# Performance work log

Hardware: AMD Instinct MI355X
Metric: run time of the kernel (lower is better)

The kernel has to match this reference:

```python
import jax, jax.numpy as jnp
import numpy as np

N_HEAD = 16

def setup_inputs() -> dict:
    key = jax.random.key(0)
    k1, k2, k3, k4 = jax.random.split(key, 4)
    B, S, D = 4, 1024, 1024
    x = jax.random.normal(k1, (B, S, D), dtype=jnp.float32)
    # 0/1 float mask: cls_mask[:,0] overrides row 0, cls_mask[:,1] overrides col 0
    cls_mask = jax.random.randint(k2, (B, 2, S), 0, 2).astype(jnp.float32)
    w_attn = jax.random.normal(k3, (D, 3 * D), dtype=jnp.float32) * 0.02
    b_attn = jnp.zeros((3 * D,), dtype=jnp.float32)
    w_proj = jax.random.normal(k4, (D, D), dtype=jnp.float32) * 0.02
    b_proj = jnp.zeros((D,), dtype=jnp.float32)
    return {"x": x, "cls_mask": cls_mask, "w_attn": w_attn, "b_attn": b_attn,
            "w_proj": w_proj, "b_proj": b_proj}

def reference(x, cls_mask, w_attn, b_attn, w_proj, b_proj):
    B, S, D = x.shape
    H = N_HEAD
    hd = D // H
    cm = jnp.broadcast_to(jnp.tril(jnp.ones((S, S), x.dtype))[None, None], (B, 1, S, S))
    cm = cm.at[:, :, 0, :].set(cls_mask[:, 0][:, None, :])
    cm = cm.at[:, :, :, 0].set(cls_mask[:, 1][:, None, :])
    qkv = x @ w_attn + b_attn                      # [B,S,3D]
    q, k, v = jnp.split(qkv, 3, axis=-1)
    split_heads = lambda t: t.reshape(B, S, H, hd).transpose(0, 2, 1, 3)  # [B,H,S,hd]
    q, k, v = split_heads(q), split_heads(k), split_heads(v)
    w = jnp.einsum('bhqd,bhkd->bhqk', q, k) / jnp.sqrt(jnp.asarray(hd, x.dtype))
    w = w * cm - 10000.0 * (1.0 - cm)
    w = jax.nn.softmax(w, axis=-1)
    a = jnp.einsum('bhqk,bhkd->bhqd', w, v)
    a = a.transpose(0, 2, 1, 3).reshape(B, S, D)   # merge heads
    a = a @ w_proj + b_proj
    present = jnp.stack((k, v))                    # [2,B,H,S,hd]
    return a, present
```

## Files before the change

kernel.cpp:

```cpp
#include <hip/hip_runtime.h>
#include <hip/hip_bf16.h>

typedef __bf16 bf16x8 __attribute__((ext_vector_type(8)));
typedef float f32x4 __attribute__((ext_vector_type(4)));

__device__ __forceinline__ f32x4 mfma16(bf16x8 a, bf16x8 b, f32x4 c) {
    return __builtin_amdgcn_mfma_f32_16x16x32_bf16(a, b, c, 0, 0, 0);
}

typedef __attribute__((address_space(1))) const unsigned int GUInt;
typedef __attribute__((address_space(3))) unsigned int LUInt;
__device__ __forceinline__ void gl_lds16(const void* g, void* l) {
    __builtin_amdgcn_global_load_lds((GUInt*)g, (LUInt*)l, 16, 0, 0);
}

__device__ __forceinline__ int psw(int row, int bir) {
    return row * 128 + (bir ^ ((row & 7) << 4));
}

__global__ __launch_bounds__(256) void cast_kernel(const float* __restrict__ in,
                                                   __hip_bfloat16* __restrict__ out, int n4) {
    int i = blockIdx.x * 256 + threadIdx.x;
    if (i >= n4) return;
    float4 v = reinterpret_cast<const float4*>(in)[i];
    __hip_bfloat16 o[4];
    o[0] = __float2bfloat16(v.x); o[1] = __float2bfloat16(v.y);
    o[2] = __float2bfloat16(v.z); o[3] = __float2bfloat16(v.w);
    *reinterpret_cast<uint2*>(&out[i * 4]) = *reinterpret_cast<const uint2*>(o);
}

__global__ __launch_bounds__(256) void transpose_cast_kernel(const float* __restrict__ in,
                                                             __hip_bfloat16* __restrict__ out,
                                                             int K, int N) {
    __shared__ float tile[64][65];
    int kt = blockIdx.x, nt = blockIdx.y;
    int c = threadIdx.x & 63, r4 = threadIdx.x >> 6;
#pragma unroll
    for (int i = 0; i < 16; ++i) {
        int r = i * 4 + r4;
        tile[r][c] = in[(kt * 64 + r) * N + nt * 64 + c];
    }
    __syncthreads();
#pragma unroll
    for (int i = 0; i < 16; ++i) {
        int rr = i * 4 + r4;
        out[(nt * 64 + rr) * K + kt * 64 + c] = __float2bfloat16(tile[c][rr]);
    }
}

template <int EPI>
__global__ __launch_bounds__(256) void gemm_kernel(
    const __hip_bfloat16* __restrict__ A, const __hip_bfloat16* __restrict__ Bt,
    const float* __restrict__ bias, int M, int N, int K,
    float* __restrict__ Cf,
    __hip_bfloat16* __restrict__ Qbf, __hip_bfloat16* __restrict__ Kbf,
    __hip_bfloat16* __restrict__ VbfT, float* __restrict__ present) {
    __shared__ __align__(16) char As[128 * 128];
    __shared__ __align__(16) char Bs[128 * 128];
    const int tid = threadIdx.x;
    const int lane = tid & 63;
    const int w = tid >> 6;
    const int lr = lane & 15;
    const int lg = lane >> 4;
    const int wm = (w >> 1) * 64;
    const int wn = (w & 1) * 64;
    const int bm = blockIdx.y, bn = blockIdx.x;
    const int swz = (lr & 7) << 4;

    const int srow = tid >> 3;
    const int ccs = ((tid & 7) * 16) ^ ((srow & 7) << 4);
    const char* aBase = (const char*)A + ((size_t)(bm * 128 + srow) * K) * 2 + ccs;
    const char* bBase = (const char*)Bt + ((size_t)(bn * 128 + srow) * K) * 2 + ccs;

    f32x4 zv = {0.f, 0.f, 0.f, 0.f};
    f32x4 acc[4][4];
#pragma unroll
    for (int i = 0; i < 4; ++i)
#pragma unroll
        for (int j = 0; j < 4; ++j) acc[i][j] = zv;

    for (int k0 = 0; k0 < K; k0 += 64) {
#pragma unroll
        for (int j = 0; j < 4; ++j) {
            gl_lds16(aBase + ((size_t)j * 32 * K + k0) * 2, &As[j * 4096 + tid * 16]);
            gl_lds16(bBase + ((size_t)j * 32 * K + k0) * 2, &Bs[j * 4096 + tid * 16]);
        }
        __syncthreads();
#pragma unroll
        for (int kk = 0; kk < 2; ++kk) {
            bf16x8 af[4], bfr[4];
#pragma unroll
            for (int mt = 0; mt < 4; ++mt)
                af[mt] = *reinterpret_cast<const bf16x8*>(
                    &As[(wm + mt * 16 + lr) * 128 + ((kk * 64 + lg * 16) ^ swz)]);
#pragma unroll
            for (int nt = 0; nt < 4; ++nt)
                bfr[nt] = *reinterpret_cast<const bf16x8*>(
                    &Bs[(wn + nt * 16 + lr) * 128 + ((kk * 64 + lg * 16) ^ swz)]);
#pragma unroll
            for (int mt = 0; mt < 4; ++mt)
#pragma unroll
                for (int nt = 0; nt < 4; ++nt)
                    acc[mt][nt] = mfma16(af[mt], bfr[nt], acc[mt][nt]);
        }
        __syncthreads();
    }

#pragma unroll
    for (int mt = 0; mt < 4; ++mt) {
        const int mbase = bm * 128 + wm + mt * 16 + lg * 4;
        const int bb = mbase >> 10, s0 = mbase & 1023;
#pragma unroll
        for (int nt = 0; nt < 4; ++nt) {
            const int n = bn * 128 + wn + nt * 16 + lr;
            const float bias_n = bias[n];
            float v[4];
#pragma unroll
            for (int r = 0; r < 4; ++r) v[r] = acc[mt][nt][r] + bias_n;
            if (EPI == 0) {
#pragma unroll
                for (int r = 0; r < 4; ++r) Cf[(size_t)(mbase + r) * N + n] = v[r];
            } else {
                const int sec = n >> 10, nn = n & 1023;
                const int hh = nn >> 6, d = nn & 63;
                const int rowbase = ((bb * 16 + hh) * 1024 + s0) * 64 + d;
                if (sec == 0) {
#pragma unroll
                    for (int r = 0; r < 4; ++r) Qbf[rowbase + r * 64] = __float2bfloat16(v[r]);
                } else if (sec == 1) {
#pragma unroll
                    for (int r = 0; r < 4; ++r) {
                        Kbf[rowbase + r * 64] = __float2bfloat16(v[r]);
                        present[rowbase + r * 64] = v[r];
                    }
                } else {
                    __hip_bfloat16 pk[4];
#pragma unroll
                    for (int r = 0; r < 4; ++r) {
                        pk[r] = __float2bfloat16(v[r]);
                        present[4194304 + rowbase + r * 64] = v[r];
                    }
                    *reinterpret_cast<uint2*>(&VbfT[((bb * 16 + hh) * 64 + d) * 1024 + s0]) =
                        *reinterpret_cast<const uint2*>(pk);
                }
            }
        }
    }
}

__global__ __launch_bounds__(256) void attn_kernel(
    const __hip_bfloat16* __restrict__ Qbf, const __hip_bfloat16* __restrict__ Kbf,
    const __hip_bfloat16* __restrict__ VbfT, const float* __restrict__ cls,
    __hip_bfloat16* __restrict__ Abf) {
    __shared__ __align__(16) char KV[2][16384];
    __shared__ __align__(16) char P_lds[4 * 2048];
    const int tid = threadIdx.x;
    const int lane = tid & 63;
    const int w = tid >> 6;
    const int lr = lane & 15;
    const int lg = lane >> 4;
    const int lk = lg * 8;
    const int qx = blockIdx.x, h = blockIdx.y, b = blockIdx.z;
    const int qt = (qx == 0) ? 15 : ((qx == 1) ? 0 : 16 - qx);
    const int bh = b * 16 + h;
    const int qbase = qt * 64 + w * 16;
    char* Pw = &P_lds[w * 2048];
    const int ntiles = (qt == 0) ? 16 : (qt + 1);

    const char* kSrc = (const char*)Kbf + (size_t)bh * 131072;
    const char* vSrc = (const char*)VbfT + (size_t)bh * 131072;
    const int srow = tid >> 3;
    const int ccs = ((tid & 7) * 16) ^ ((srow & 7) << 4);

#define STAGE(BUF, T)                                                          \
    do {                                                                       \
        const int kv0s_ = (T) * 64;                                            \
        char* dst_ = &KV[BUF][tid * 16];                                       \
        gl_lds16(kSrc + (size_t)(kv0s_ + srow) * 128 + ccs, dst_);             \
        gl_lds16(kSrc + (size_t)(kv0s_ + 32 + srow) * 128 + ccs, dst_ + 4096); \
        gl_lds16(vSrc + (size_t)srow * 2048 + kv0s_ * 2 + ccs, dst_ + 8192);   \
        gl_lds16(vSrc + (size_t)(32 + srow) * 2048 + kv0s_ * 2 + ccs, dst_ + 12288); \
    } while (0)

    STAGE(0, 0);

    bf16x8 aq[2];
#pragma unroll
    for (int c = 0; c < 2; ++c)
        aq[c] = *reinterpret_cast<const bf16x8*>(&Qbf[(size_t)(bh * 1024 + qbase + lr) * 64 + c * 32 + lk]);

    float clscol[4];
#pragma unroll
    for (int r = 0; r < 4; ++r)
        clscol[r] = cls[b * 2048 + 1024 + qbase + lg * 4 + r];

    bf16x8 ones;
#pragma unroll
    for (int i = 0; i < 8; ++i) ones[i] = (__bf16)1.0f;

    const float SC = 0.125f * 1.44269504088896f;
    f32x4 zv = {0.f, 0.f, 0.f, 0.f};
    f32x4 acc_o[4];
    f32x4 acc_l = zv;
#pragma unroll
    for (int i = 0; i < 4; ++i) acc_o[i] = zv;

    const int swz = (lr & 7) << 4;
    __syncthreads();

    int buf = 0;
    for (int t = 0; t < ntiles; ++t) {
        if (t + 1 < ntiles) STAGE(buf ^ 1, t + 1);
        const char* Kb = KV[buf];
        const char* Vb = KV[buf] + 8192;
        const int kv0 = t * 64;

        float clsrow[4] = {1.f, 1.f, 1.f, 1.f};
        if (qt == 0 && w == 0) {
#pragma unroll
            for (int nt = 0; nt < 4; ++nt) clsrow[nt] = cls[b * 2048 + kv0 + nt * 16 + lr];
        }

        f32x4 sacc[4];
#pragma unroll
        for (int nt = 0; nt < 4; ++nt) {
            const char* kr = Kb + (nt * 16 + lr) * 128;
            bf16x8 k0 = *reinterpret_cast<const bf16x8*>(kr + ((lg * 16) ^ swz));
            bf16x8 k1 = *reinterpret_cast<const bf16x8*>(kr + ((64 + lg * 16) ^ swz));
            sacc[nt] = mfma16(aq[1], k1, mfma16(aq[0], k0, zv));
        }

        float p[4][4];
#pragma unroll
        for (int nt = 0; nt < 4; ++nt) {
            int k_j = kv0 + nt * 16 + lr;
#pragma unroll
            for (int r = 0; r < 4; ++r) {
                int q_i = qbase + lg * 4 + r;
                float e = __builtin_amdgcn_exp2f(sacc[nt][r] * SC);
                bool keep = (k_j <= q_i);
                if (q_i == 0) keep = (clsrow[nt] != 0.f);
                if (k_j == 0) keep = (clscol[r] != 0.f);
                p[nt][r] = keep ? e : 0.f;
            }
        }

#pragma unroll
        for (int nt = 0; nt < 4; ++nt)
#pragma unroll
            for (int r = 0; r < 4; ++r)
                *reinterpret_cast<__hip_bfloat16*>(&Pw[psw(lg * 4 + r, nt * 32 + lr * 2)]) =
                    __float2bfloat16(p[nt][r]);
        bf16x8 pa0 = *reinterpret_cast<const bf16x8*>(&Pw[psw(lr, lk * 2)]);
        bf16x8 pa1 = *reinterpret_cast<const bf16x8*>(&Pw[psw(lr, 64 + lk * 2)]);

        acc_l = mfma16(pa1, ones, mfma16(pa0, ones, acc_l));

#pragma unroll
        for (int ntd = 0; ntd < 4; ++ntd) {
            const char* vr = Vb + (ntd * 16 + lr) * 128;
            bf16x8 v0 = *reinterpret_cast<const bf16x8*>(vr + ((lg * 16) ^ swz));
            bf16x8 v1 = *reinterpret_cast<const bf16x8*>(vr + ((64 + lg * 16) ^ swz));
            acc_o[ntd] = mfma16(pa1, v1, mfma16(pa0, v0, acc_o[ntd]));
        }
        __syncthreads();
        buf ^= 1;
    }
#undef STAGE

#pragma unroll
    for (int r = 0; r < 4; ++r) {
        float inv = 1.f / acc_l[r];
        int q_i = qbase + lg * 4 + r;
#pragma unroll
        for (int ntd = 0; ntd < 4; ++ntd) {
            int dd = ntd * 16 + lr;
            Abf[(size_t)(b * 1024 + q_i) * 1024 + h * 64 + dd] = __float2bfloat16(acc_o[ntd][r] * inv);
        }
    }
}

extern "C" void kernel_launch(void* const* d_in, const int* in_sizes, int n_in,
                              void* d_out, int out_size, void* d_ws, size_t ws_size,
                              hipStream_t stream) {
    const float* x      = (const float*)d_in[0];
    const float* cls    = (const float*)d_in[1];
    const float* w_attn = (const float*)d_in[2];
    const float* b_attn = (const float*)d_in[3];
    const float* w_proj = (const float*)d_in[4];
    const float* b_proj = (const float*)d_in[5];
    float* out_a = (float*)d_out;
    float* present = out_a + 4194304;

    char* ws = (char*)d_ws;
    __hip_bfloat16* Xbf    = (__hip_bfloat16*)(ws);
    __hip_bfloat16* Abf    = (__hip_bfloat16*)(ws);
    __hip_bfloat16* WattnT = (__hip_bfloat16*)(ws + 12ull * 1024 * 1024);
    __hip_bfloat16* WprojT = (__hip_bfloat16*)(ws + 20ull * 1024 * 1024);
    __hip_bfloat16* Qbf    = (__hip_bfloat16*)(ws + 24ull * 1024 * 1024);
    __hip_bfloat16* Kbf    = (__hip_bfloat16*)(ws + 36ull * 1024 * 1024);
    __hip_bfloat16* VbfT   = (__hip_bfloat16*)(ws + 48ull * 1024 * 1024);

    cast_kernel<<<4096, 256, 0, stream>>>(x, Xbf, 1048576);
    transpose_cast_kernel<<<dim3(16, 48), 256, 0, stream>>>(w_attn, WattnT, 1024, 3072);
    transpose_cast_kernel<<<dim3(16, 16), 256, 0, stream>>>(w_proj, WprojT, 1024, 1024);
    gemm_kernel<1><<<dim3(24, 32), 256, 0, stream>>>(Xbf, WattnT, b_attn, 4096, 3072, 1024,
                                                     nullptr, Qbf, Kbf, VbfT, present);
    attn_kernel<<<dim3(16, 16, 4), 256, 0, stream>>>(Qbf, Kbf, VbfT, cls, Abf);
    gemm_kernel<0><<<dim3(8, 32), 256, 0, stream>>>(Abf, WprojT, b_proj, 4096, 1024, 1024,
                                                    out_a, nullptr, nullptr, nullptr, nullptr);
}
```

Baseline: 115.9 us.

## Pair causal query tiles per block, split CLS row into separate kernel, merge prep kernels

Each attention block now handles two query tiles (a and 15-a) so that every block does the same total amount of causal work and shares the staged K/V tiles between them. The special CLS row 0, which previously forced tile 0 to scan all keys, moves to a small dedicated kernel. This keeps the per-block causal loop free of the CLS-row branch. The three cast/transpose launches are fused into one prep kernel to cut launch overhead. The cost is more registers per block (two accumulator states), which may lower occupancy, and half as many attention blocks.

Measured after the change: 117.3 us. No clear change (+1.2%).

```diff
diff --git a/kernel.cpp b/kernel.cpp
--- a/kernel.cpp
+++ b/kernel.cpp
@@ -18,33 +18,37 @@
     return row * 128 + (bir ^ ((row & 7) << 4));
 }
 
-__global__ __launch_bounds__(256) void cast_kernel(const float* __restrict__ in,
-                                                   __hip_bfloat16* __restrict__ out, int n4) {
-    int i = blockIdx.x * 256 + threadIdx.x;
-    if (i >= n4) return;
-    float4 v = reinterpret_cast<const float4*>(in)[i];
-    __hip_bfloat16 o[4];
-    o[0] = __float2bfloat16(v.x); o[1] = __float2bfloat16(v.y);
-    o[2] = __float2bfloat16(v.z); o[3] = __float2bfloat16(v.w);
-    *reinterpret_cast<uint2*>(&out[i * 4]) = *reinterpret_cast<const uint2*>(o);
-}
-
-__global__ __launch_bounds__(256) void transpose_cast_kernel(const float* __restrict__ in,
-                                                             __hip_bfloat16* __restrict__ out,
-                                                             int K, int N) {
+__global__ __launch_bounds__(256) void prep_kernel(
+    const float* __restrict__ x, __hip_bfloat16* __restrict__ Xbf,
+    const float* __restrict__ w_attn, __hip_bfloat16* __restrict__ WattnT,
+    const float* __restrict__ w_proj, __hip_bfloat16* __restrict__ WprojT) {
     __shared__ float tile[64][65];
-    int kt = blockIdx.x, nt = blockIdx.y;
-    int c = threadIdx.x & 63, r4 = threadIdx.x >> 6;
+    const int bid = blockIdx.x;
+    const int tid = threadIdx.x;
+    if (bid < 4096) {
+        int i = bid * 256 + tid;
+        float4 v = reinterpret_cast<const float4*>(x)[i];
+        __hip_bfloat16 o[4];
+        o[0] = __float2bfloat16(v.x); o[1] = __float2bfloat16(v.y);
+        o[2] = __float2bfloat16(v.z); o[3] = __float2bfloat16(v.w);
+        *reinterpret_cast<uint2*>(&Xbf[i * 4]) = *reinterpret_cast<const uint2*>(o);
+        return;
+    }
+    const float* in; __hip_bfloat16* out; int K, N, t;
+    if (bid < 4096 + 768) { t = bid - 4096; in = w_attn; out = WattnT; K = 1024; N = 3072; }
+    else                  { t = bid - 4864; in = w_proj; out = WprojT; K = 1024; N = 1024; }
+    const int kt = t & 15, nt = t >> 4;
+    const int c = tid & 63, r4 = tid >> 6;
 #pragma unroll
     for (int i = 0; i < 16; ++i) {
         int r = i * 4 + r4;
-        tile[r][c] = in[(kt * 64 + r) * N + nt * 64 + c];
+        tile[r][c] = in[(size_t)(kt * 64 + r) * N + nt * 64 + c];
     }
     __syncthreads();
 #pragma unroll
     for (int i = 0; i < 16; ++i) {
         int rr = i * 4 + r4;
-        out[(nt * 64 + rr) * K + kt * 64 + c] = __float2bfloat16(tile[c][rr]);
+        out[(size_t)(nt * 64 + rr) * K + kt * 64 + c] = __float2bfloat16(tile[c][rr]);
     }
 }
 
@@ -148,6 +152,89 @@
     }
 }
 
+struct AttnState {
+    bf16x8 aq[2];
+    float clscol[4];
+    f32x4 acc_o[4];
+    f32x4 acc_l;
+    int qbase;
+};
+
+__device__ __forceinline__ void attn_init(
+    AttnState& st, const __hip_bfloat16* Qbf, const float* cls,
+    int bh, int b, int qt, int w, int lr, int lg) {
+    st.qbase = qt * 64 + w * 16;
+#pragma unroll
+    for (int c = 0; c < 2; ++c)
+        st.aq[c] = *reinterpret_cast<const bf16x8*>(
+            &Qbf[(size_t)(bh * 1024 + st.qbase + lr) * 64 + c * 32 + lg * 8]);
+#pragma unroll
+    for (int r = 0; r < 4; ++r)
+        st.clscol[r] = cls[b * 2048 + 1024 + st.qbase + lg * 4 + r];
+    f32x4 zv = {0.f, 0.f, 0.f, 0.f};
+    st.acc_l = zv;
+#pragma unroll
+    for (int i = 0; i < 4; ++i) st.acc_o[i] = zv;
+}
+
+__device__ __forceinline__ void attn_tile(
+    AttnState& st, const char* Kb, const char* Vb, int kv0,
+    char* Pw, int lr, int lg, int lk, int swz, bf16x8 ones, float SC) {
+    f32x4 zv = {0.f, 0.f, 0.f, 0.f};
+    f32x4 sacc[4];
+#pragma unroll
+    for (int nt = 0; nt < 4; ++nt) {
+        const char* kr = Kb + (nt * 16 + lr) * 128;
+        bf16x8 k0 = *reinterpret_cast<const bf16x8*>(kr + ((lg * 16) ^ swz));
+        bf16x8 k1 = *reinterpret_cast<const bf16x8*>(kr + ((64 + lg * 16) ^ swz));
+        sacc[nt] = mfma16(st.aq[1], k1, mfma16(st.aq[0], k0, zv));
+    }
+    float p[4][4];
+#pragma unroll
+    for (int nt = 0; nt < 4; ++nt) {
+        int k_j = kv0 + nt * 16 + lr;
+#pragma unroll
+        for (int r = 0; r < 4; ++r) {
+            int q_i = st.qbase + lg * 4 + r;
+            float e = __builtin_amdgcn_exp2f(sacc[nt][r] * SC);
+            bool keep = (k_j <= q_i);
+            if (k_j == 0) keep = (st.clscol[r] != 0.f);
+            p[nt][r] = keep ? e : 0.f;
+        }
+    }
+#pragma unroll
+    for (int nt = 0; nt < 4; ++nt)
+#pragma unroll
+        for (int r = 0; r < 4; ++r)
+            *reinterpret_cast<__hip_bfloat16*>(&Pw[psw(lg * 4 + r, nt * 32 + lr * 2)]) =
+                __float2bfloat16(p[nt][r]);
+    bf16x8 pa0 = *reinterpret_cast<const bf16x8*>(&Pw[psw(lr, lk * 2)]);
+    bf16x8 pa1 = *reinterpret_cast<const bf16x8*>(&Pw[psw(lr, 64 + lk * 2)]);
+    st.acc_l = mfma16(pa1, ones, mfma16(pa0, ones, st.acc_l));
+#pragma unroll
+    for (int ntd = 0; ntd < 4; ++ntd) {
+        const char* vr = Vb + (ntd * 16 + lr) * 128;
+        bf16x8 v0 = *reinterpret_cast<const bf16x8*>(vr + ((lg * 16) ^ swz));
+        bf16x8 v1 = *reinterpret_cast<const bf16x8*>(vr + ((64 + lg * 16) ^ swz));
+        st.acc_o[ntd] = mfma16(pa1, v1, mfma16(pa0, v0, st.acc_o[ntd]));
+    }
+}
+
+__device__ __forceinline__ void attn_store(
+    const AttnState& st, __hip_bfloat16* Abf, int b, int h, int lr, int lg) {
+#pragma unroll
+    for (int r = 0; r < 4; ++r) {
+        float inv = 1.f / st.acc_l[r];
+        int q_i = st.qbase + lg * 4 + r;
+#pragma unroll
+        for (int ntd = 0; ntd < 4; ++ntd) {
+            int dd = ntd * 16 + lr;
+            Abf[(size_t)(b * 1024 + q_i) * 1024 + h * 64 + dd] =
+                __float2bfloat16(st.acc_o[ntd][r] * inv);
+        }
+    }
+}
+
 __global__ __launch_bounds__(256) void attn_kernel(
     const __hip_bfloat16* __restrict__ Qbf, const __hip_bfloat16* __restrict__ Kbf,
     const __hip_bfloat16* __restrict__ VbfT, const float* __restrict__ cls,
@@ -160,12 +247,11 @@
     const int lr = lane & 15;
     const int lg = lane >> 4;
     const int lk = lg * 8;
-    const int qx = blockIdx.x, h = blockIdx.y, b = blockIdx.z;
-    const int qt = (qx == 0) ? 15 : ((qx == 1) ? 0 : 16 - qx);
+    const int a = blockIdx.x, h = blockIdx.y, b = blockIdx.z;
     const int bh = b * 16 + h;
-    const int qbase = qt * 64 + w * 16;
     char* Pw = &P_lds[w * 2048];
-    const int ntiles = (qt == 0) ? 16 : (qt + 1);
+    const int nlo = a + 1;
+    const int nhi = 16 - a;
 
     const char* kSrc = (const char*)Kbf + (size_t)bh * 131072;
     const char* vSrc = (const char*)VbfT + (size_t)bh * 131072;
@@ -184,99 +270,86 @@
 
     STAGE(0, 0);
 
-    bf16x8 aq[2];
-#pragma unroll
-    for (int c = 0; c < 2; ++c)
-        aq[c] = *reinterpret_cast<const bf16x8*>(&Qbf[(size_t)(bh * 1024 + qbase + lr) * 64 + c * 32 + lk]);
-
-    float clscol[4];
-#pragma unroll
-    for (int r = 0; r < 4; ++r)
-        clscol[r] = cls[b * 2048 + 1024 + qbase + lg * 4 + r];
+    AttnState lo, hi;
+    attn_init(lo, Qbf, cls, bh, b, a, w, lr, lg);
+    attn_init(hi, Qbf, cls, bh, b, 15 - a, w, lr, lg);
 
     bf16x8 ones;
 #pragma unroll
     for (int i = 0; i < 8; ++i) ones[i] = (__bf16)1.0f;
-
     const float SC = 0.125f * 1.44269504088896f;
-    f32x4 zv = {0.f, 0.f, 0.f, 0.f};
-    f32x4 acc_o[4];
-    f32x4 acc_l = zv;
-#pragma unroll
-    for (int i = 0; i < 4; ++i) acc_o[i] = zv;
-
     const int swz = (lr & 7) << 4;
     __syncthreads();
 
     int buf = 0;
-    for (int t = 0; t < ntiles; ++t) {
-        if (t + 1 < ntiles) STAGE(buf ^ 1, t + 1);
+    for (int t = 0; t < nhi; ++t) {
+        if (t + 1 < nhi) STAGE(buf ^ 1, t + 1);
         const char* Kb = KV[buf];
         const char* Vb = KV[buf] + 8192;
-        const int kv0 = t * 64;
-
-        float clsrow[4] = {1.f, 1.f, 1.f, 1.f};
-        if (qt == 0 && w == 0) {
-#pragma unroll
-            for (int nt = 0; nt < 4; ++nt) clsrow[nt] = cls[b * 2048 + kv0 + nt * 16 + lr];
-        }
-
-        f32x4 sacc[4];
-#pragma unroll
-        for (int nt = 0; nt < 4; ++nt) {
-            const char* kr = Kb + (nt * 16 + lr) * 128;
-            bf16x8 k0 = *reinterpret_cast<const bf16x8*>(kr + ((lg * 16) ^ swz));
-            bf16x8 k1 = *reinterpret_cast<const bf16x8*>(kr + ((64 + lg * 16) ^ swz));
-            sacc[nt] = mfma16(aq[1], k1, mfma16(aq[0], k0, zv));
-        }
-
-        float p[4][4];
-#pragma unroll
-        for (int nt = 0; nt < 4; ++nt) {
-            int k_j = kv0 + nt * 16 + lr;
-#pragma unroll
-            for (int r = 0; r < 4; ++r) {
-                int q_i = qbase + lg * 4 + r;
-                float e = __builtin_amdgcn_exp2f(sacc[nt][r] * SC);
-                bool keep = (k_j <= q_i);
-                if (q_i == 0) keep = (clsrow[nt] != 0.f);
-                if (k_j == 0) keep = (clscol[r] != 0.f);
-                p[nt][r] = keep ? e : 0.f;
-            }
-        }
-
-#pragma unroll
-        for (int nt = 0; nt < 4; ++nt)
-#pragma unroll
-            for (int r = 0; r < 4; ++r)
-                *reinterpret_cast<__hip_bfloat16*>(&Pw[psw(lg * 4 + r, nt * 32 + lr * 2)]) =
-                    __float2bfloat16(p[nt][r]);
-        bf16x8 pa0 = *reinterpret_cast<const bf16x8*>(&Pw[psw(lr, lk * 2)]);
-        bf16x8 pa1 = *reinterpret_cast<const bf16x8*>(&Pw[psw(lr, 64 + lk * 2)]);
-
-        acc_l = mfma16(pa1, ones, mfma16(pa0, ones, acc_l));
-
-#pragma unroll
-        for (int ntd = 0; ntd < 4; ++ntd) {
-            const char* vr = Vb + (ntd * 16 + lr) * 128;
-            bf16x8 v0 = *reinterpret_cast<const bf16x8*>(vr + ((lg * 16) ^ swz));
-            bf16x8 v1 = *reinterpret_cast<const bf16x8*>(vr + ((64 + lg * 16) ^ swz));
-            acc_o[ntd] = mfma16(pa1, v1, mfma16(pa0, v0, acc_o[ntd]));
-        }
+        attn_tile(hi, Kb, Vb, t * 64, Pw, lr, lg, lk, swz, ones, SC);
+        if (t < nlo) attn_tile(lo, Kb, Vb, t * 64, Pw, lr, lg, lk, swz, ones, SC);
         __syncthreads();
         buf ^= 1;
     }
 #undef STAGE
 
-#pragma unroll
-    for (int r = 0; r < 4; ++r) {
-        float inv = 1.f / acc_l[r];
-        int q_i = qbase + lg * 4 + r;
-#pragma unroll
-        for (int ntd = 0; ntd < 4; ++ntd) {
-            int dd = ntd * 16 + lr;
-            Abf[(size_t)(b * 1024 + q_i) * 1024 + h * 64 + dd] = __float2bfloat16(acc_o[ntd][r] * inv);
-        }
+    attn_store(lo, Abf, b, h, lr, lg);
+    attn_store(hi, Abf, b, h, lr, lg);
+}
+
+__global__ __launch_bounds__(256) void cls_row_kernel(
+    const __hip_bfloat16* __restrict__ Qbf, const __hip_bfloat16* __restrict__ Kbf,
+    const __hip_bfloat16* __restrict__ VbfT, const float* __restrict__ cls,
+    __hip_bfloat16* __restrict__ Abf) {
+    __shared__ float q_sh[64];
+    __shared__ float p_sh[1024];
+    __shared__ float l_sh[4];
+    __shared__ float o_sh[4][64];
+    const int h = blockIdx.x, b = blockIdx.y;
+    const int bh = b * 16 + h;
+    const int tid = threadIdx.x, w = tid >> 6, lane = tid & 63;
+    const float SC = 0.125f * 1.44269504088896f;
+
+    if (tid < 64) q_sh[tid] = __bfloat162float(Qbf[(size_t)bh * 65536 + tid]);
+    __syncthreads();
+
+    float lpart = 0.f;
+#pragma unroll
+    for (int jj = 0; jj < 4; ++jj) {
+        const int j = tid * 4 + jj;
+        const bf16x8* krow = reinterpret_cast<const bf16x8*>(&Kbf[(size_t)bh * 65536 + j * 64]);
+        float s = 0.f;
+#pragma unroll
+        for (int c = 0; c < 8; ++c) {
+            bf16x8 k8 = krow[c];
+#pragma unroll
+            for (int e = 0; e < 8; ++e) s += q_sh[c * 8 + e] * (float)k8[e];
+        }
+        bool keep = (cls[b * 2048 + j] != 0.f);
+        if (j == 0) keep = (cls[b * 2048 + 1024] != 0.f);
+        float pj = keep ? __builtin_amdgcn_exp2f(s * SC) : 0.f;
+        p_sh[j] = pj;
+        lpart += pj;
+    }
+#pragma unroll
+    for (int off = 32; off >= 1; off >>= 1) lpart += __shfl_xor(lpart, off);
+    if (lane == 0) l_sh[w] = lpart;
+    __syncthreads();
+    const float l = l_sh[0] + l_sh[1] + l_sh[2] + l_sh[3];
+
+    float od = 0.f;
+    const __hip_bfloat16* vrow = &VbfT[(size_t)bh * 65536 + (size_t)lane * 1024 + w * 256];
+#pragma unroll 8
+    for (int c = 0; c < 32; ++c) {
+        bf16x8 v8 = *reinterpret_cast<const bf16x8*>(&vrow[c * 8]);
+#pragma unroll
+        for (int e = 0; e < 8; ++e) od += p_sh[w * 256 + c * 8 + e] * (float)v8[e];
+    }
+    o_sh[w][lane] = od;
+    __syncthreads();
+    if (tid < 64) {
+        float o = (o_sh[0][tid] + o_sh[1][tid] + o_sh[2][tid] + o_sh[3][tid]) / l;
+        Abf[(size_t)b * 1048576 + h * 64 + tid] = __float2bfloat16(o);
     }
 }
 
@@ -301,12 +374,11 @@
     __hip_bfloat16* Kbf    = (__hip_bfloat16*)(ws + 36ull * 1024 * 1024);
     __hip_bfloat16* VbfT   = (__hip_bfloat16*)(ws + 48ull * 1024 * 1024);
 
-    cast_kernel<<<4096, 256, 0, stream>>>(x, Xbf, 1048576);
-    transpose_cast_kernel<<<dim3(16, 48), 256, 0, stream>>>(w_attn, WattnT, 1024, 3072);
-    transpose_cast_kernel<<<dim3(16, 16), 256, 0, stream>>>(w_proj, WprojT, 1024, 1024);
+    prep_kernel<<<5120, 256, 0, stream>>>(x, Xbf, w_attn, WattnT, w_proj, WprojT);
     gemm_kernel<1><<<dim3(24, 32), 256, 0, stream>>>(Xbf, WattnT, b_attn, 4096, 3072, 1024,
                                                      nullptr, Qbf, Kbf, VbfT, present);
-    attn_kernel<<<dim3(16, 16, 4), 256, 0, stream>>>(Qbf, Kbf, VbfT, cls, Abf);
+    attn_kernel<<<dim3(8, 16, 4), 256, 0, stream>>>(Qbf, Kbf, VbfT, cls, Abf);
+    cls_row_kernel<<<dim3(16, 4), 256, 0, stream>>>(Qbf, Kbf, VbfT, cls, Abf);
     gemm_kernel<0><<<dim3(8, 32), 256, 0, stream>>>(Abf, WprojT, b_proj, 4096, 1024, 1024,
                                                     out_a, nullptr, nullptr, nullptr, nullptr);
 }
```
